# Kernel tuning notes

Hardware: AMD Instinct MI355X
Metric: run time of the kernel (lower is better)

## Reference

```python
import jax, jax.numpy as jnp
import numpy as np

B, T, H, V = 32, 256, 1024, 256


def setup_inputs() -> dict:
    key = jax.random.key(0)
    ks = jax.random.split(key, 12)
    xavier = float(np.sqrt(6.0 / (H + V)))
    inp = {
        "x": jax.random.randint(ks[0], (B, T), 0, V, dtype=jnp.int64),
        "targets": jax.random.randint(ks[1], (B, T), 0, V, dtype=jnp.int64),
        "h0": jnp.zeros((B, H), jnp.float32),
        "c0": jnp.zeros((B, H), jnp.float32),
        "h1": jnp.zeros((B, H), jnp.float32),
        "c1": jnp.zeros((B, H), jnp.float32),
        # learned params
        "emb": jax.random.normal(ks[2], (V, H), jnp.float32) * 0.05,
        "W_ih0": jax.random.normal(ks[3], (H, 4 * H), jnp.float32) / np.sqrt(H),
        "W_hh0": jax.random.normal(ks[4], (H, 4 * H), jnp.float32) / np.sqrt(H),
        "b0": jnp.zeros((4 * H,), jnp.float32),
        "W_ih1": jax.random.normal(ks[5], (H, 4 * H), jnp.float32) / np.sqrt(H),
        "W_hh1": jax.random.normal(ks[6], (H, 4 * H), jnp.float32) / np.sqrt(H),
        "b1": jnp.zeros((4 * H,), jnp.float32),
        "W_out": jax.random.uniform(ks[7], (H, V), jnp.float32, -xavier, xavier),
        "b_out": jnp.zeros((V,), jnp.float32),
    }
    return inp


def _lstm_cell(h, c, inp, W_ih, W_hh, b):
    # gates: [B, 4H] -> i, f, g, o
    z = inp @ W_ih + h @ W_hh + b
    i, f, g, o = jnp.split(z, 4, axis=-1)
    c_new = jax.nn.sigmoid(f) * c + jax.nn.sigmoid(i) * jnp.tanh(g)
    h_new = jax.nn.sigmoid(o) * jnp.tanh(c_new)
    return h_new, c_new


def reference(x, targets, h0, c0, h1, c1, emb, W_ih0, W_hh0, b0,
              W_ih1, W_hh1, b1, W_out, b_out):
    # Teacher-forcing branch: embed targets, feed embedding at every step.
    embeddings = emb[targets]            # [B, T, H]
    e_seq = jnp.swapaxes(embeddings, 0, 1)  # [T, B, H] for scan over time

    def step(carry, e_t):
        (h0, c0), (h1, c1) = carry
        h0, c0 = _lstm_cell(h0, c0, e_t, W_ih0, W_hh0, b0)
        h1, c1 = _lstm_cell(h1, c1, h0, W_ih1, W_hh1, b1)
        logit = h1 @ W_out + b_out       # [B, V]
        return ((h0, c0), (h1, c1)), logit

    carry0 = ((h0, c0), (h1, c1))
    carry_f, logits_tbv = jax.lax.scan(step, carry0, e_seq)
    logits = jnp.swapaxes(logits_tbv, 0, 1)  # [B, T, V]
    (h0f, c0f), (h1f, c1f) = carry_f
    return logits, h0f, c0f, h1f, c1f
```

## Files before the change

kernel.cpp:

```cpp
#include <hip/hip_runtime.h>
#include <cstdint>


typedef float    f32x4 __attribute__((ext_vector_type(4)));
typedef short    s16x8 __attribute__((ext_vector_type(8)));
typedef unsigned u32x4 __attribute__((ext_vector_type(4)));

#define DEV __device__ __forceinline__

DEV unsigned short f2bf(float x){
  unsigned u = __builtin_bit_cast(unsigned, x);
  unsigned r = (u + 0x7fffu + ((u >> 16) & 1u)) >> 16;
  return (unsigned short)r;
}
DEV float bf2f(unsigned short b){ return __builtin_bit_cast(float, ((unsigned)b) << 16); }

DEV s16x8 ld16(const void* p){ return *(const s16x8*)p; }

DEV f32x4 MF(s16x8 a, s16x8 b, f32x4 c){
  return __builtin_amdgcn_mfma_f32_16x16x32_bf16(a, b, c, 0, 0, 0);
}

#define LDC(dst, ptr)  asm volatile("global_load_dwordx4 %0, %1, off sc0 sc1" : "=v"(dst) : "v"(ptr))
#define LDP(dst, ptr)  asm volatile("global_load_dwordx4 %0, %1, off"         : "=v"(dst) : "v"(ptr))
#define WAITVM(n) do { asm volatile("s_waitcnt vmcnt(" #n ")" ::: "memory"); \
                       __builtin_amdgcn_sched_barrier(0); } while (0)
#define CFENCE()  asm volatile("" ::: "memory")
#define TRIPLE(Cmn, Ahm, Alm, Bhn, Bln) do { \
    Cmn = MF(Ahm, Bhn, Cmn); Cmn = MF(Ahm, Bln, Cmn); Cmn = MF(Alm, Bhn, Cmn); } while (0)

DEV void st16c(void* p, u32x4 v){
  asm volatile("global_store_dwordx4 %0, %1, off sc0 sc1" :: "v"(p), "v"(v) : "memory");
}
DEV void set_flag(int* p, int v){
  __hip_atomic_store(p, v, __ATOMIC_RELAXED, __HIP_MEMORY_SCOPE_AGENT);
}
template<int SLP>
DEV void pollT(const int* f, int lane, int target){
  const int* p0 = f + lane * 8;
  const int* p1 = f + (64 + lane) * 8;
  for (;;) {
    int a = __hip_atomic_load(p0, __ATOMIC_RELAXED, __HIP_MEMORY_SCOPE_AGENT);
    int b = __hip_atomic_load(p1, __ATOMIC_RELAXED, __HIP_MEMORY_SCOPE_AGENT);
    if (__all((a >= target) && (b >= target))) break;
    __builtin_amdgcn_s_sleep(SLP);
  }
  CFENCE();
}
DEV char* h0slot(char* wa0, char* s0, char* hi, int s){
  return (s == 0) ? s0 : ((s <= 128) ? wa0 + ((size_t)(s - 1) << 17)
                                     : hi  + ((size_t)(s - 129) << 17));
}

DEV void halfgemm8(const char* smemMat, const char* ALb, const char* Bb,
                   int wgl, int ksb, int lane, f32x4 (&C)[2][2]) {
  s16x8 P[3][4], AL[3][2];
  #pragma unroll
  for (int d = 0; d < 2; ++d) {
    #pragma unroll
    for (int q = 0; q < 4; ++q) LDP(P[d][q], Bb + ((q * 32 + ksb + d) << 10) + lane * 16);
    LDP(AL[d][0], ALb + ((((wgl * 2 + 0) * 2 + 1) * 32 + ksb + d) << 10) + lane * 16);
    LDP(AL[d][1], ALb + ((((wgl * 2 + 1) * 2 + 1) * 32 + ksb + d) << 10) + lane * 16);
  }
  #pragma unroll
  for (int i = 0; i < 8; ++i) {
    const int ks = ksb + i;
    if (i < 6) {
      #pragma unroll
      for (int q = 0; q < 4; ++q) LDP(P[(i + 2) % 3][q], Bb + ((q * 32 + ks + 2) << 10) + lane * 16);
      LDP(AL[(i + 2) % 3][0], ALb + ((((wgl * 2 + 0) * 2 + 1) * 32 + ks + 2) << 10) + lane * 16);
      LDP(AL[(i + 2) % 3][1], ALb + ((((wgl * 2 + 1) * 2 + 1) * 32 + ks + 2) << 10) + lane * 16);
    }
    s16x8 Ah0 = ld16(smemMat + ((0 * 32 + ks) << 10) + lane * 16);
    s16x8 Ah1 = ld16(smemMat + ((1 * 32 + ks) << 10) + lane * 16);
    if (i < 6) { WAITVM(12); } else if (i == 6) { WAITVM(6); } else { WAITVM(0); }
    TRIPLE(C[0][0], Ah0, AL[i % 3][0], P[i % 3][0], P[i % 3][2]);
    TRIPLE(C[0][1], Ah0, AL[i % 3][0], P[i % 3][1], P[i % 3][3]);
    TRIPLE(C[1][0], Ah1, AL[i % 3][1], P[i % 3][0], P[i % 3][2]);
    TRIPLE(C[1][1], Ah1, AL[i % 3][1], P[i % 3][1], P[i % 3][3]);
  }
}

__global__ void prep_wfrag(const float* __restrict__ W0, const float* __restrict__ W1,
                           const float* __restrict__ W2, const float* __restrict__ W3,
                           char* D0, char* D1, char* D2, char* D3) {
  int gid = blockIdx.x * 256 + threadIdx.x;
  int lane = gid & 63, ks = (gid >> 6) & 31, jb = (gid >> 11) & 255, mat = gid >> 19;
  const float* S = (mat == 0) ? W0 : (mat == 1) ? W1 : (mat == 2) ? W2 : W3;
  char* D = (mat == 0) ? D0 : (mat == 1) ? D1 : (mat == 2) ? D2 : D3;
  int jp = jb * 16 + (lane & 15), u = jp >> 2, g = jp & 3;
  int kb = ks * 32 + (lane >> 4) * 8;
  s16x8 vh, vl;
  #pragma unroll
  for (int i = 0; i < 8; ++i) {
    float x = S[(kb + i) * 4096 + g * 1024 + u];
    unsigned short h = f2bf(x);
    vh[i] = (short)h;
    vl[i] = (short)f2bf(x - bf2f(h));
  }
  *(s16x8*)(D + (((jb * 2 + 0) * 32 + ks) << 10) + lane * 16) = vh;
  *(s16x8*)(D + (((jb * 2 + 1) * 32 + ks) << 10) + lane * 16) = vl;
}

__global__ void prep_bfrag(const float* __restrict__ emb, const float* __restrict__ Wout,
                           char* Demb, char* Dwout) {
  int gid = blockIdx.x * 256 + threadIdx.x;
  int lane = gid & 63, ks = (gid >> 6) & 31, vb = (gid >> 11) & 15, which = gid >> 15;
  int v = vb * 16 + (lane & 15), kb = ks * 32 + (lane >> 4) * 8;
  s16x8 vh, vl;
  #pragma unroll
  for (int i = 0; i < 8; ++i) {
    float x = which ? Wout[(kb + i) * 256 + v] : emb[v * 1024 + kb + i];
    unsigned short h = f2bf(x);
    vh[i] = (short)h;
    vl[i] = (short)f2bf(x - bf2f(h));
  }
  char* D = which ? Dwout : Demb;
  *(s16x8*)(D + (((vb * 2 + 0) * 32 + ks) << 10) + lane * 16) = vh;
  *(s16x8*)(D + (((vb * 2 + 1) * 32 + ks) << 10) + lane * 16) = vl;
}

__global__ void prep_hinit(const float* __restrict__ h0, const float* __restrict__ h1,
                           char* h0s0, char* h1f) {
  int gid = blockIdx.x * 256 + threadIdx.x;
  int lane = gid & 63, ks = (gid >> 6) & 31, nt = (gid >> 11) & 1, which = gid >> 12;
  const float* S = which ? h1 : h0;
  char* D = which ? h1f : h0s0;
  int b = nt * 16 + (lane & 15), kb = ks * 32 + (lane >> 4) * 8;
  s16x8 vh, vl;
  #pragma unroll
  for (int i = 0; i < 8; ++i) {
    float x = S[b * 1024 + kb + i];
    unsigned short h = f2bf(x);
    vh[i] = (short)h;
    vl[i] = (short)f2bf(x - bf2f(h));
  }
  *(s16x8*)(D + (((0 * 2 + nt) * 32 + ks) << 10) + lane * 16) = vh;
  *(s16x8*)(D + (((1 * 2 + nt) * 32 + ks) << 10) + lane * 16) = vl;
}

__global__ void prep_misc(const float* __restrict__ b1, float* b1i, int* f0a, int* f1a) {
  int i = blockIdx.x * 256 + threadIdx.x;
  if (i < 4096) b1i[i] = b1[(i & 3) * 1024 + (i >> 2)];
  if (i < 1024) { f0a[i] = -1; f1a[i] = -1; }
}

__global__ __launch_bounds__(256, 1) void lstm_persist(
    const int* __restrict__ tgt,
    const float* __restrict__ c0_in, const float* __restrict__ c1_in,
    const float* __restrict__ b0, const float* __restrict__ b_out,
    char* __restrict__ WA0, const char* __restrict__ WA1, const char* __restrict__ WA2,
    const char* __restrict__ WAi0, const char* __restrict__ WoutB, const char* __restrict__ embB,
    float* __restrict__ E0, const float* __restrict__ b1i,
    char* __restrict__ h0s0, char* __restrict__ h0hi, char* __restrict__ h1frag,
    int* __restrict__ f0, int* __restrict__ f1,
    float* __restrict__ out)
{
  extern __shared__ char smem[];
  constexpr int PART = 131072;
  constexpr int RP   = 131072 + 16384;
  const int tid = threadIdx.x, lane = tid & 63, wv = tid >> 6;
  const int wg = blockIdx.x;
  const bool isL0 = (wg < 128);
  const int wgl = isL0 ? wg : (wg - 128);
  const int l15 = lane & 15, l4 = lane >> 4;
  const int mi_e = wv >> 1, nt_e = wv & 1;

  __builtin_amdgcn_fence(__ATOMIC_ACQUIRE, "agent");

  if (isL0) {
    u32x4 tmp[8];
    for (int blk = 0; blk < 4; ++blk) {
      #pragma unroll
      for (int q = 0; q < 8; ++q) {
        int idx = tid + (blk * 8 + q) * 256;
        int l16 = idx & 63, ks = (idx >> 6) & 31, mi = (idx >> 11) & 1, part = idx >> 12;
        LDC(tmp[q], WA0 + ((((wgl * 2 + mi) * 2 + part) * 32 + ks) << 10) + l16 * 16);
      }
      WAITVM(0);
      #pragma unroll
      for (int q = 0; q < 8; ++q) {
        int idx = tid + (blk * 8 + q) * 256;
        int l16 = idx & 63, ks = (idx >> 6) & 31, mi = (idx >> 11) & 1, part = idx >> 12;
        *(u32x4*)(smem + (((part * 2 + mi) * 32 + ks) << 10) + l16 * 16) = tmp[q];
      }
    }
  } else {
    for (int idx = tid; idx < 8192; idx += 256) {
      int l16 = idx & 63, ks = (idx >> 6) & 31, mi = (idx >> 11) & 1, mat = idx >> 12;
      const char* W = mat ? WA2 : WA1;
      u32x4 v = *(const u32x4*)(W + ((((wgl * 2 + mi) * 2 + 0) * 32 + ks) << 10) + l16 * 16);
      *(u32x4*)(smem + (((mat * 2 + mi) * 32 + ks) << 10) + l16 * 16) = v;
    }
  }

  if (isL0) {
    f32x4 C[2][4];
    #pragma unroll
    for (int a = 0; a < 2; ++a)
      #pragma unroll
      for (int b = 0; b < 4; ++b) C[a][b] = 0.0f;
    for (int ks = 0; ks < 32; ++ks) {
      s16x8 Ah0, Ah1, Al0, Al1;
      LDC(Ah0, WAi0 + ((((wgl * 2 + 0) * 2 + 0) * 32 + ks) << 10) + lane * 16);
      LDC(Ah1, WAi0 + ((((wgl * 2 + 1) * 2 + 0) * 32 + ks) << 10) + lane * 16);
      LDC(Al0, WAi0 + ((((wgl * 2 + 0) * 2 + 1) * 32 + ks) << 10) + lane * 16);
      LDC(Al1, WAi0 + ((((wgl * 2 + 1) * 2 + 1) * 32 + ks) << 10) + lane * 16);
      WAITVM(0);
      #pragma unroll
      for (int v4 = 0; v4 < 4; ++v4) {
        int vb = wv * 4 + v4;
        s16x8 Bh = ld16(embB + (((vb * 2 + 0) * 32 + ks) << 10) + lane * 16);
        s16x8 Bl = ld16(embB + (((vb * 2 + 1) * 32 + ks) << 10) + lane * 16);
        TRIPLE(C[0][v4], Ah0, Al0, Bh, Bl);
        TRIPLE(C[1][v4], Ah1, Al1, Bh, Bl);
      }
    }
    #pragma unroll
    for (int mi = 0; mi < 2; ++mi) {
      int jb4 = wgl * 32 + mi * 16 + l4 * 4;
      int u = jb4 >> 2;
      f32x4 bb;
      #pragma unroll
      for (int r = 0; r < 4; ++r) bb[r] = b0[r * 1024 + u];
      #pragma unroll
      for (int v4 = 0; v4 < 4; ++v4) {
        int v = (wv * 4 + v4) * 16 + l15;
        *(f32x4*)(E0 + v * 4096 + jb4) = C[mi][v4] + bb;
      }
    }
  }

  float cst;
  {
    const float* cs = isL0 ? c0_in : c1_in;
    cst = cs[(nt_e * 16 + l15) * 1024 + wgl * 8 + mi_e * 4 + l4];
  }
  f32x4 b1z = {0.f, 0.f, 0.f, 0.f};
  if (!isL0) b1z = *(const f32x4*)(b1i + wgl * 32 + mi_e * 16 + (l4 << 2));

  __syncthreads();
  if (tid == 0) set_flag((isL0 ? f0 : f1) + wgl * 8, 0);

  if (isL0) {
    for (int t = 0; t < 256; ++t) {
      const int s = t + 1;
      f32x4 C[2][2];
      #pragma unroll
      for (int a = 0; a < 2; ++a)
        #pragma unroll
        for (int b = 0; b < 2; ++b) C[a][b] = 0.0f;

      int tv = tgt[(nt_e * 16 + l15) * 256 + t];
      f32x4 e0v = *(const f32x4*)(E0 + (size_t)tv * 4096 + wgl * 32 + mi_e * 16 + (l4 << 2));
      pollT<1>(f0, lane, t);
      const char* Bb = h0slot(WA0, h0s0, h0hi, t);
      const int ksb = wv * 8;
      s16x8 P[3][4];
      #pragma unroll
      for (int d = 0; d < 2; ++d)
        #pragma unroll
        for (int q = 0; q < 4; ++q) LDP(P[d][q], Bb + ((q * 32 + ksb + d) << 10) + lane * 16);
      #pragma unroll
      for (int i = 0; i < 8; ++i) {
        const int ks = ksb + i;
        if (i < 6) {
          #pragma unroll
          for (int q = 0; q < 4; ++q) LDP(P[(i + 2) % 3][q], Bb + ((q * 32 + ks + 2) << 10) + lane * 16);
        }
        s16x8 Ah0 = ld16(smem + ((0 * 32 + ks) << 10) + lane * 16);
        s16x8 Ah1 = ld16(smem + ((1 * 32 + ks) << 10) + lane * 16);
        s16x8 Al0 = ld16(smem + ((2 * 32 + ks) << 10) + lane * 16);
        s16x8 Al1 = ld16(smem + ((3 * 32 + ks) << 10) + lane * 16);
        if (i < 6) { WAITVM(8); } else if (i == 6) { WAITVM(4); } else { WAITVM(0); }
        TRIPLE(C[0][0], Ah0, Al0, P[i % 3][0], P[i % 3][2]);
        TRIPLE(C[0][1], Ah0, Al0, P[i % 3][1], P[i % 3][3]);
        TRIPLE(C[1][0], Ah1, Al1, P[i % 3][0], P[i % 3][2]);
        TRIPLE(C[1][1], Ah1, Al1, P[i % 3][1], P[i % 3][3]);
      }

      #pragma unroll
      for (int mi = 0; mi < 2; ++mi)
        #pragma unroll
        for (int nt = 0; nt < 2; ++nt)
          *(f32x4*)(smem + PART + ((wv * 4 + mi * 2 + nt) << 10) + lane * 16) = C[mi][nt];
      __syncthreads();

      {
        f32x4 z = *(const f32x4*)(smem + PART + ((0 * 4 + wv) << 10) + lane * 16);
        #pragma unroll
        for (int w = 1; w < 4; ++w)
          z += *(const f32x4*)(smem + PART + ((w * 4 + wv) << 10) + lane * 16);
        z += e0v;
        float ig = 1.f / (1.f + __expf(-z[0]));
        float fg = 1.f / (1.f + __expf(-z[1]));
        float og = 1.f / (1.f + __expf(-z[3]));
        float cn = fg * cst + ig * tanhf(z[2]);
        float hn = og * tanhf(cn);
        cst = cn;
        unsigned short hb = f2bf(hn);
        unsigned short lb = f2bf(hn - bf2f(hb));
        *(short*)(smem + RP + ((0 + nt_e) * 16 + l15) * 16 + (mi_e * 4 + l4) * 2) = (short)hb;
        *(short*)(smem + RP + ((2 + nt_e) * 16 + l15) * 16 + (mi_e * 4 + l4) * 2) = (short)lb;
        if (t == 255) {
          int u = wgl * 8 + mi_e * 4 + l4, b = nt_e * 16 + l15;
          out[2097152 + b * 1024 + u] = hn;
          out[2097152 + 32768 + b * 1024 + u] = cn;
        }
      }
      __syncthreads();

      if (wv == 0) {
        char* hd = h0slot(WA0, h0s0, h0hi, s);
        u32x4 v = *(const u32x4*)(smem + RP + lane * 16);
        char* dst = hd + (((lane >> 4) * 32 + (wgl >> 2)) << 10) + ((wgl & 3) * 16 + l15) * 16;
        st16c(dst, v);
        asm volatile("s_waitcnt vmcnt(0)" ::: "memory");
        if (lane == 0) set_flag(f0 + wgl * 8, s);
      }
    }
  } else {
    f32x4 zpre;
    {
      pollT<2>(f0, lane, 1);
      f32x4 C2[2][2];
      #pragma unroll
      for (int a = 0; a < 2; ++a)
        #pragma unroll
        for (int b = 0; b < 2; ++b) C2[a][b] = 0.0f;
      halfgemm8(smem, WA1, h0slot(WA0, h0s0, h0hi, 1), wgl, wv * 8, lane, C2);
      #pragma unroll
      for (int mi = 0; mi < 2; ++mi)
        #pragma unroll
        for (int nt = 0; nt < 2; ++nt)
          *(f32x4*)(smem + PART + ((wv * 4 + mi * 2 + nt) << 10) + lane * 16) = C2[mi][nt];
      __syncthreads();
      zpre = *(const f32x4*)(smem + PART + ((0 * 4 + wv) << 10) + lane * 16);
      #pragma unroll
      for (int w = 1; w < 4; ++w)
        zpre += *(const f32x4*)(smem + PART + ((w * 4 + wv) << 10) + lane * 16);
      __syncthreads();
    }

    for (int t = 0; t < 256; ++t) {
      const int s = t + 1;
      f32x4 C[2][2];
      #pragma unroll
      for (int a = 0; a < 2; ++a)
        #pragma unroll
        for (int b = 0; b < 2; ++b) C[a][b] = 0.0f;

      pollT<1>(f1, lane, t);
      halfgemm8(smem + 65536, WA2, h1frag + (size_t)t * 131072, wgl, wv * 8, lane, C);

      #pragma unroll
      for (int mi = 0; mi < 2; ++mi)
        #pragma unroll
        for (int nt = 0; nt < 2; ++nt)
          *(f32x4*)(smem + PART + ((wv * 4 + mi * 2 + nt) << 10) + lane * 16) = C[mi][nt];
      __syncthreads();

      {
        f32x4 z = *(const f32x4*)(smem + PART + ((0 * 4 + wv) << 10) + lane * 16);
        #pragma unroll
        for (int w = 1; w < 4; ++w)
          z += *(const f32x4*)(smem + PART + ((w * 4 + wv) << 10) + lane * 16);
        z += zpre + b1z;
        float ig = 1.f / (1.f + __expf(-z[0]));
        float fg = 1.f / (1.f + __expf(-z[1]));
        float og = 1.f / (1.f + __expf(-z[3]));
        float cn = fg * cst + ig * tanhf(z[2]);
        float hn = og * tanhf(cn);
        cst = cn;
        unsigned short hb = f2bf(hn);
        unsigned short lb = f2bf(hn - bf2f(hb));
        *(short*)(smem + RP + ((0 + nt_e) * 16 + l15) * 16 + (mi_e * 4 + l4) * 2) = (short)hb;
        *(short*)(smem + RP + ((2 + nt_e) * 16 + l15) * 16 + (mi_e * 4 + l4) * 2) = (short)lb;
        if (t == 255) {
          int u = wgl * 8 + mi_e * 4 + l4, b = nt_e * 16 + l15;
          out[2097152 + 65536 + b * 1024 + u] = hn;
          out[2097152 + 65536 + 32768 + b * 1024 + u] = cn;
        }
      }
      __syncthreads();

      if (wv == 0) {
        char* hd = h1frag + (size_t)s * 131072;
        u32x4 v = *(const u32x4*)(smem + RP + lane * 16);
        char* dst = hd + (((lane >> 4) * 32 + (wgl >> 2)) << 10) + ((wgl & 3) * 16 + l15) * 16;
        st16c(dst, v);
        asm volatile("s_waitcnt vmcnt(0)" ::: "memory");
        if (lane == 0) set_flag(f1 + wgl * 8, s);
      }

      if (t < 255) {
        pollT<2>(f0, lane, t + 2);
        f32x4 C2[2][2];
        #pragma unroll
        for (int a = 0; a < 2; ++a)
          #pragma unroll
          for (int b = 0; b < 2; ++b) C2[a][b] = 0.0f;
        halfgemm8(smem, WA1, h0slot(WA0, h0s0, h0hi, t + 2), wgl, wv * 8, lane, C2);
        #pragma unroll
        for (int mi = 0; mi < 2; ++mi)
          #pragma unroll
          for (int nt = 0; nt < 2; ++nt)
            *(f32x4*)(smem + PART + ((wv * 4 + mi * 2 + nt) << 10) + lane * 16) = C2[mi][nt];
        __syncthreads();
        zpre = *(const f32x4*)(smem + PART + ((0 * 4 + wv) << 10) + lane * 16);
        #pragma unroll
        for (int w = 1; w < 4; ++w)
          zpre += *(const f32x4*)(smem + PART + ((w * 4 + wv) << 10) + lane * 16);
        __syncthreads();
      }
    }
  }

  {
    const int tp = isL0 ? wgl : (128 + wgl);
    pollT<32>(f1, lane, tp + 1);
    const char* A = h1frag + (size_t)(tp + 1) * 131072;
    f32x4 C[2][4];
    #pragma unroll
    for (int a = 0; a < 2; ++a)
      #pragma unroll
      for (int b = 0; b < 4; ++b) C[a][b] = 0.0f;
    s16x8 QA[4], QB[4];
    #pragma unroll
    for (int q = 0; q < 4; ++q) LDP(QA[q], A + ((q * 32 + 0) << 10) + lane * 16);
    for (int kk = 0; kk < 16; ++kk) {
      const int ks = kk * 2;
      #pragma unroll
      for (int q = 0; q < 4; ++q) LDP(QB[q], A + ((q * 32 + ks + 1) << 10) + lane * 16);
      asm volatile("s_waitcnt vmcnt(4)" ::: "memory");
      __builtin_amdgcn_sched_barrier(0);
      #pragma unroll
      for (int v4 = 0; v4 < 4; ++v4) {
        int vb = wv * 4 + v4;
        s16x8 Bh = ld16(WoutB + (((vb * 2 + 0) * 32 + ks) << 10) + lane * 16);
        s16x8 Bl = ld16(WoutB + (((vb * 2 + 1) * 32 + ks) << 10) + lane * 16);
        C[0][v4] = MF(QA[0], Bh, C[0][v4]); C[0][v4] = MF(QA[0], Bl, C[0][v4]); C[0][v4] = MF(QA[2], Bh, C[0][v4]);
        C[1][v4] = MF(QA[1], Bh, C[1][v4]); C[1][v4] = MF(QA[1], Bl, C[1][v4]); C[1][v4] = MF(QA[3], Bh, C[1][v4]);
      }
      if (kk < 15) {
        #pragma unroll
        for (int q = 0; q < 4; ++q) LDP(QA[q], A + ((q * 32 + ks + 2) << 10) + lane * 16);
        asm volatile("s_waitcnt vmcnt(4)" ::: "memory");
      } else {
        asm volatile("s_waitcnt vmcnt(0)" ::: "memory");
      }
      __builtin_amdgcn_sched_barrier(0);
      #pragma unroll
      for (int v4 = 0; v4 < 4; ++v4) {
        int vb = wv * 4 + v4;
        s16x8 Bh = ld16(WoutB + (((vb * 2 + 0) * 32 + ks + 1) << 10) + lane * 16);
        s16x8 Bl = ld16(WoutB + (((vb * 2 + 1) * 32 + ks + 1) << 10) + lane * 16);
        C[0][v4] = MF(QB[0], Bh, C[0][v4]); C[0][v4] = MF(QB[0], Bl, C[0][v4]); C[0][v4] = MF(QB[2], Bh, C[0][v4]);
        C[1][v4] = MF(QB[1], Bh, C[1][v4]); C[1][v4] = MF(QB[1], Bl, C[1][v4]); C[1][v4] = MF(QB[3], Bh, C[1][v4]);
      }
    }
    #pragma unroll
    for (int nt = 0; nt < 2; ++nt)
      #pragma unroll
      for (int v4 = 0; v4 < 4; ++v4) {
        int v = (wv * 4 + v4) * 16 + l15;
        float bo = b_out[v];
        #pragma unroll
        for (int r = 0; r < 4; ++r) {
          int b = nt * 16 + l4 * 4 + r;
          out[((size_t)b * 256 + tp) * 256 + v] = C[nt][v4][r] + bo;
        }
      }
  }
}

extern "C" void kernel_launch(void* const* d_in, const int* in_sizes, int n_in,
                              void* d_out, int out_size, void* d_ws, size_t ws_size,
                              hipStream_t stream) {
  const int*   targets = (const int*)d_in[1];
  const float* h0_in   = (const float*)d_in[2];
  const float* c0_in   = (const float*)d_in[3];
  const float* h1_in   = (const float*)d_in[4];
  const float* c1_in   = (const float*)d_in[5];
  const float* emb     = (const float*)d_in[6];
  const float* W_ih0   = (const float*)d_in[7];
  const float* W_hh0   = (const float*)d_in[8];
  const float* b0      = (const float*)d_in[9];
  const float* W_ih1   = (const float*)d_in[10];
  const float* W_hh1   = (const float*)d_in[11];
  const float* b1      = (const float*)d_in[12];
  const float* W_out   = (const float*)d_in[13];
  const float* b_out   = (const float*)d_in[14];
  float* out = (float*)d_out;

  char* ws = (char*)d_ws;
  char*  WA0    = ws;
  char*  WA1    = ws + 16777216;
  char*  WA2    = ws + 33554432;
  char*  WoutB  = ws + 50331648;
  char*  embB   = ws + 51380224;
  float* E0     = (float*)(ws + 52428800);
  float* b1i    = (float*)(ws + 56623104);
  int*   f0     = (int*)(ws + 56639488);
  int*   f1     = (int*)(ws + 56643584);
  char*  h0s0   = ws + 56647680;
  char*  h0hi   = ws + 56778752;
  char*  h1frag = ws + 73555968;
  char*  WAi0   = h1frag + 16777216;

  prep_misc <<<18,   256, 0, stream>>>(b1, b1i, f0, f1);
  prep_wfrag<<<8192, 256, 0, stream>>>(W_hh0, W_ih1, W_hh1, W_ih0, WA0, WA1, WA2, WAi0);
  prep_bfrag<<<256,  256, 0, stream>>>(emb, W_out, embB, WoutB);
  prep_hinit<<<32,   256, 0, stream>>>(h0_in, h1_in, h0s0, h1frag);

  hipFuncSetAttribute(reinterpret_cast<const void*>(lstm_persist),
                      hipFuncAttributeMaxDynamicSharedMemorySize, 148480);
  lstm_persist<<<256, 256, 148480, stream>>>(
      targets, c0_in, c1_in, b0, b_out,
      WA0, WA1, WA2, WAi0, WoutB, embB,
      E0, b1i, h0s0, h0hi, h1frag, f0, f1, out);
}
```

Baseline: 1.729 ms.

## Split layer-1 into separate input-projection and recurrent workgroup groups with ring buffer

Layer-1 work previously done by 128 workgroups is split into two groups of 64. One group computes the W_ih1·h0 projection and pushes partial gate sums into a 4-slot global ring. The other group computes the W_hh1·h1 recurrence, adds the ring entry and runs the cell update. Each workgroup now handles 16 gate rows via a wider gemm16u, and a new flag array f2 plus combined polls coordinate the stages. The aim is to take the input projection off the layer-1 recurrent critical path. In exchange it adds global traffic for the ring, more cross-workgroup polling, and serialises the activation step on a single wave.

```diff
diff --git a/kernel.cpp b/kernel.cpp
--- a/kernel.cpp
+++ b/kernel.cpp
@@ -32,6 +32,7 @@
 DEV void st16c(void* p, u32x4 v){
   asm volatile("global_store_dwordx4 %0, %1, off sc0 sc1" :: "v"(p), "v"(v) : "memory");
 }
+DEV void st16cf(void* p, f32x4 v){ st16c(p, __builtin_bit_cast(u32x4, v)); }
 DEV void set_flag(int* p, int v){
   __hip_atomic_store(p, v, __ATOMIC_RELAXED, __HIP_MEMORY_SCOPE_AGENT);
 }
@@ -47,20 +48,48 @@
   }
   CFENCE();
 }
+DEV void pollC(const int* f1p, int t1, const int* f2p, int t2, int lane){
+  const int* a = f1p + lane * 8;
+  const int* b = f2p + lane * 8;
+  for (;;) {
+    int x = __hip_atomic_load(a, __ATOMIC_RELAXED, __HIP_MEMORY_SCOPE_AGENT);
+    int y = __hip_atomic_load(b, __ATOMIC_RELAXED, __HIP_MEMORY_SCOPE_AGENT);
+    if (__all((x >= t1) && (y >= t2))) break;
+    __builtin_amdgcn_s_sleep(1);
+  }
+  CFENCE();
+}
+DEV void pollB(const int* f0p, int t0, const int* f2p, int t2,
+               const int* f1p, int t1, int lane){
+  const int* a0 = f0p + lane * 8;
+  const int* a1 = f0p + (64 + lane) * 8;
+  const int* b  = f2p + lane * 8;
+  const int* c  = f1p + lane * 8;
+  for (;;) {
+    int x0 = __hip_atomic_load(a0, __ATOMIC_RELAXED, __HIP_MEMORY_SCOPE_AGENT);
+    int x1 = __hip_atomic_load(a1, __ATOMIC_RELAXED, __HIP_MEMORY_SCOPE_AGENT);
+    int y  = __hip_atomic_load(b,  __ATOMIC_RELAXED, __HIP_MEMORY_SCOPE_AGENT);
+    int z  = __hip_atomic_load(c,  __ATOMIC_RELAXED, __HIP_MEMORY_SCOPE_AGENT);
+    if (__all((x0 >= t0) && (x1 >= t0) && (y >= t2) && (z >= t1))) break;
+    __builtin_amdgcn_s_sleep(2);
+  }
+  CFENCE();
+}
 DEV char* h0slot(char* wa0, char* s0, char* hi, int s){
   return (s == 0) ? s0 : ((s <= 128) ? wa0 + ((size_t)(s - 1) << 17)
                                      : hi  + ((size_t)(s - 129) << 17));
 }
 
-DEV void halfgemm8(const char* smemMat, const char* ALb, const char* Bb,
-                   int wgl, int ksb, int lane, f32x4 (&C)[2][2]) {
-  s16x8 P[3][4], AL[3][2];
+DEV void gemm16u(const char* smemA, const char* ALb, int jb0, const char* Bb,
+                 int ksb, int lane, f32x4 (&C)[4][2]) {
+  s16x8 P[3][4], AL[3][4];
   #pragma unroll
   for (int d = 0; d < 2; ++d) {
     #pragma unroll
     for (int q = 0; q < 4; ++q) LDP(P[d][q], Bb + ((q * 32 + ksb + d) << 10) + lane * 16);
-    LDP(AL[d][0], ALb + ((((wgl * 2 + 0) * 2 + 1) * 32 + ksb + d) << 10) + lane * 16);
-    LDP(AL[d][1], ALb + ((((wgl * 2 + 1) * 2 + 1) * 32 + ksb + d) << 10) + lane * 16);
+    #pragma unroll
+    for (int m = 0; m < 4; ++m)
+      LDP(AL[d][m], ALb + ((((jb0 + m) * 2 + 1) * 32 + ksb + d) << 10) + lane * 16);
   }
   #pragma unroll
   for (int i = 0; i < 8; ++i) {
@@ -68,16 +97,19 @@
     if (i < 6) {
       #pragma unroll
       for (int q = 0; q < 4; ++q) LDP(P[(i + 2) % 3][q], Bb + ((q * 32 + ks + 2) << 10) + lane * 16);
-      LDP(AL[(i + 2) % 3][0], ALb + ((((wgl * 2 + 0) * 2 + 1) * 32 + ks + 2) << 10) + lane * 16);
-      LDP(AL[(i + 2) % 3][1], ALb + ((((wgl * 2 + 1) * 2 + 1) * 32 + ks + 2) << 10) + lane * 16);
-    }
-    s16x8 Ah0 = ld16(smemMat + ((0 * 32 + ks) << 10) + lane * 16);
-    s16x8 Ah1 = ld16(smemMat + ((1 * 32 + ks) << 10) + lane * 16);
-    if (i < 6) { WAITVM(12); } else if (i == 6) { WAITVM(6); } else { WAITVM(0); }
-    TRIPLE(C[0][0], Ah0, AL[i % 3][0], P[i % 3][0], P[i % 3][2]);
-    TRIPLE(C[0][1], Ah0, AL[i % 3][0], P[i % 3][1], P[i % 3][3]);
-    TRIPLE(C[1][0], Ah1, AL[i % 3][1], P[i % 3][0], P[i % 3][2]);
-    TRIPLE(C[1][1], Ah1, AL[i % 3][1], P[i % 3][1], P[i % 3][3]);
+      #pragma unroll
+      for (int m = 0; m < 4; ++m)
+        LDP(AL[(i + 2) % 3][m], ALb + ((((jb0 + m) * 2 + 1) * 32 + ks + 2) << 10) + lane * 16);
+    }
+    s16x8 Ah[4];
+    #pragma unroll
+    for (int m = 0; m < 4; ++m) Ah[m] = ld16(smemA + ((m * 32 + ks) << 10) + lane * 16);
+    if (i < 6) { WAITVM(16); } else if (i == 6) { WAITVM(8); } else { WAITVM(0); }
+    #pragma unroll
+    for (int m = 0; m < 4; ++m) {
+      TRIPLE(C[m][0], Ah[m], AL[i % 3][m], P[i % 3][0], P[i % 3][2]);
+      TRIPLE(C[m][1], Ah[m], AL[i % 3][m], P[i % 3][1], P[i % 3][3]);
+    }
   }
 }
 
@@ -139,10 +171,15 @@
   *(s16x8*)(D + (((1 * 2 + nt) * 32 + ks) << 10) + lane * 16) = vl;
 }
 
-__global__ void prep_misc(const float* __restrict__ b1, float* b1i, int* f0a, int* f1a) {
+__global__ void prep_misc(const float* __restrict__ b1, float* b1i,
+                          int* f0a, int* f1a, int* f2a) {
   int i = blockIdx.x * 256 + threadIdx.x;
   if (i < 4096) b1i[i] = b1[(i & 3) * 1024 + (i >> 2)];
-  if (i < 1024) { f0a[i] = -1; f1a[i] = -1; }
+  if (i < 1024) {
+    f0a[i] = -1;
+    f1a[i] = (i >= 512) ? 0x7fffffff : -1;
+    f2a[i] = (i >= 512) ? 0x7fffffff : -1;
+  }
 }
 
 __global__ __launch_bounds__(256, 1) void lstm_persist(
@@ -153,96 +190,82 @@
     const char* __restrict__ WAi0, const char* __restrict__ WoutB, const char* __restrict__ embB,
     float* __restrict__ E0, const float* __restrict__ b1i,
     char* __restrict__ h0s0, char* __restrict__ h0hi, char* __restrict__ h1frag,
-    int* __restrict__ f0, int* __restrict__ f1,
+    char* __restrict__ z1ring,
+    int* __restrict__ f0, int* __restrict__ f1, int* __restrict__ f2,
     float* __restrict__ out)
 {
   extern __shared__ char smem[];
-  constexpr int PART = 131072;
-  constexpr int RP   = 131072 + 16384;
+  constexpr int PARTA = 131072;
+  constexpr int RP0   = 147456;
+  constexpr int PARTB = 131072;
+  constexpr int RP1   = 155648;
   const int tid = threadIdx.x, lane = tid & 63, wv = tid >> 6;
   const int wg = blockIdx.x;
-  const bool isL0 = (wg < 128);
-  const int wgl = isL0 ? wg : (wg - 128);
   const int l15 = lane & 15, l4 = lane >> 4;
-  const int mi_e = wv >> 1, nt_e = wv & 1;
 
   __builtin_amdgcn_fence(__ATOMIC_ACQUIRE, "agent");
 
-  if (isL0) {
-    u32x4 tmp[8];
-    for (int blk = 0; blk < 4; ++blk) {
-      #pragma unroll
-      for (int q = 0; q < 8; ++q) {
-        int idx = tid + (blk * 8 + q) * 256;
-        int l16 = idx & 63, ks = (idx >> 6) & 31, mi = (idx >> 11) & 1, part = idx >> 12;
-        LDC(tmp[q], WA0 + ((((wgl * 2 + mi) * 2 + part) * 32 + ks) << 10) + l16 * 16);
-      }
-      WAITVM(0);
-      #pragma unroll
-      for (int q = 0; q < 8; ++q) {
-        int idx = tid + (blk * 8 + q) * 256;
-        int l16 = idx & 63, ks = (idx >> 6) & 31, mi = (idx >> 11) & 1, part = idx >> 12;
-        *(u32x4*)(smem + (((part * 2 + mi) * 32 + ks) << 10) + l16 * 16) = tmp[q];
-      }
-    }
-  } else {
-    for (int idx = tid; idx < 8192; idx += 256) {
-      int l16 = idx & 63, ks = (idx >> 6) & 31, mi = (idx >> 11) & 1, mat = idx >> 12;
-      const char* W = mat ? WA2 : WA1;
-      u32x4 v = *(const u32x4*)(W + ((((wgl * 2 + mi) * 2 + 0) * 32 + ks) << 10) + l16 * 16);
-      *(u32x4*)(smem + (((mat * 2 + mi) * 32 + ks) << 10) + l16 * 16) = v;
-    }
-  }
-
-  if (isL0) {
-    f32x4 C[2][4];
-    #pragma unroll
-    for (int a = 0; a < 2; ++a)
-      #pragma unroll
-      for (int b = 0; b < 4; ++b) C[a][b] = 0.0f;
-    for (int ks = 0; ks < 32; ++ks) {
-      s16x8 Ah0, Ah1, Al0, Al1;
-      LDC(Ah0, WAi0 + ((((wgl * 2 + 0) * 2 + 0) * 32 + ks) << 10) + lane * 16);
-      LDC(Ah1, WAi0 + ((((wgl * 2 + 1) * 2 + 0) * 32 + ks) << 10) + lane * 16);
-      LDC(Al0, WAi0 + ((((wgl * 2 + 0) * 2 + 1) * 32 + ks) << 10) + lane * 16);
-      LDC(Al1, WAi0 + ((((wgl * 2 + 1) * 2 + 1) * 32 + ks) << 10) + lane * 16);
-      WAITVM(0);
-      #pragma unroll
-      for (int v4 = 0; v4 < 4; ++v4) {
-        int vb = wv * 4 + v4;
-        s16x8 Bh = ld16(embB + (((vb * 2 + 0) * 32 + ks) << 10) + lane * 16);
-        s16x8 Bl = ld16(embB + (((vb * 2 + 1) * 32 + ks) << 10) + lane * 16);
-        TRIPLE(C[0][v4], Ah0, Al0, Bh, Bl);
-        TRIPLE(C[1][v4], Ah1, Al1, Bh, Bl);
-      }
-    }
-    #pragma unroll
-    for (int mi = 0; mi < 2; ++mi) {
-      int jb4 = wgl * 32 + mi * 16 + l4 * 4;
-      int u = jb4 >> 2;
-      f32x4 bb;
-      #pragma unroll
-      for (int r = 0; r < 4; ++r) bb[r] = b0[r * 1024 + u];
-      #pragma unroll
-      for (int v4 = 0; v4 < 4; ++v4) {
-        int v = (wv * 4 + v4) * 16 + l15;
-        *(f32x4*)(E0 + v * 4096 + jb4) = C[mi][v4] + bb;
-      }
-    }
-  }
-
-  float cst;
-  {
-    const float* cs = isL0 ? c0_in : c1_in;
-    cst = cs[(nt_e * 16 + l15) * 1024 + wgl * 8 + mi_e * 4 + l4];
-  }
-  f32x4 b1z = {0.f, 0.f, 0.f, 0.f};
-  if (!isL0) b1z = *(const f32x4*)(b1i + wgl * 32 + mi_e * 16 + (l4 << 2));
-
-  __syncthreads();
-  if (tid == 0) set_flag((isL0 ? f0 : f1) + wgl * 8, 0);
-
-  if (isL0) {
+  if (wg < 128) {
+    const int wgl = wg;
+    const int mi_e = wv >> 1, nt_e = wv & 1;
+    {
+      u32x4 tmp[8];
+      for (int blk = 0; blk < 4; ++blk) {
+        #pragma unroll
+        for (int q = 0; q < 8; ++q) {
+          int idx = tid + (blk * 8 + q) * 256;
+          int l16 = idx & 63, ks = (idx >> 6) & 31, mi = (idx >> 11) & 1, part = idx >> 12;
+          LDC(tmp[q], WA0 + ((((wgl * 2 + mi) * 2 + part) * 32 + ks) << 10) + l16 * 16);
+        }
+        WAITVM(0);
+        #pragma unroll
+        for (int q = 0; q < 8; ++q) {
+          int idx = tid + (blk * 8 + q) * 256;
+          int l16 = idx & 63, ks = (idx >> 6) & 31, mi = (idx >> 11) & 1, part = idx >> 12;
+          *(u32x4*)(smem + (((part * 2 + mi) * 32 + ks) << 10) + l16 * 16) = tmp[q];
+        }
+      }
+    }
+    {
+      f32x4 C[2][4];
+      #pragma unroll
+      for (int a = 0; a < 2; ++a)
+        #pragma unroll
+        for (int b = 0; b < 4; ++b) C[a][b] = 0.0f;
+      for (int ks = 0; ks < 32; ++ks) {
+        s16x8 Ah0, Ah1, Al0, Al1;
+        LDC(Ah0, WAi0 + ((((wgl * 2 + 0) * 2 + 0) * 32 + ks) << 10) + lane * 16);
+        LDC(Ah1, WAi0 + ((((wgl * 2 + 1) * 2 + 0) * 32 + ks) << 10) + lane * 16);
+        LDC(Al0, WAi0 + ((((wgl * 2 + 0) * 2 + 1) * 32 + ks) << 10) + lane * 16);
+        LDC(Al1, WAi0 + ((((wgl * 2 + 1) * 2 + 1) * 32 + ks) << 10) + lane * 16);
+        WAITVM(0);
+        #pragma unroll
+        for (int v4 = 0; v4 < 4; ++v4) {
+          int vb = wv * 4 + v4;
+          s16x8 Bh = ld16(embB + (((vb * 2 + 0) * 32 + ks) << 10) + lane * 16);
+          s16x8 Bl = ld16(embB + (((vb * 2 + 1) * 32 + ks) << 10) + lane * 16);
+          TRIPLE(C[0][v4], Ah0, Al0, Bh, Bl);
+          TRIPLE(C[1][v4], Ah1, Al1, Bh, Bl);
+        }
+      }
+      #pragma unroll
+      for (int mi = 0; mi < 2; ++mi) {
+        int jb4 = wgl * 32 + mi * 16 + l4 * 4;
+        int u = jb4 >> 2;
+        f32x4 bb;
+        #pragma unroll
+        for (int r = 0; r < 4; ++r) bb[r] = b0[r * 1024 + u];
+        #pragma unroll
+        for (int v4 = 0; v4 < 4; ++v4) {
+          int v = (wv * 4 + v4) * 16 + l15;
+          *(f32x4*)(E0 + v * 4096 + jb4) = C[mi][v4] + bb;
+        }
+      }
+    }
+    float cst = c0_in[(nt_e * 16 + l15) * 1024 + wgl * 8 + mi_e * 4 + l4];
+    __syncthreads();
+    if (tid == 0) set_flag(f0 + wgl * 8, 0);
+
     for (int t = 0; t < 256; ++t) {
       const int s = t + 1;
       f32x4 C[2][2];
@@ -250,7 +273,6 @@
       for (int a = 0; a < 2; ++a)
         #pragma unroll
         for (int b = 0; b < 2; ++b) C[a][b] = 0.0f;
-
       int tv = tgt[(nt_e * 16 + l15) * 256 + t];
       f32x4 e0v = *(const f32x4*)(E0 + (size_t)tv * 4096 + wgl * 32 + mi_e * 16 + (l4 << 2));
       pollT<1>(f0, lane, t);
@@ -278,19 +300,17 @@
         TRIPLE(C[1][0], Ah1, Al1, P[i % 3][0], P[i % 3][2]);
         TRIPLE(C[1][1], Ah1, Al1, P[i % 3][1], P[i % 3][3]);
       }
-
       #pragma unroll
       for (int mi = 0; mi < 2; ++mi)
         #pragma unroll
         for (int nt = 0; nt < 2; ++nt)
-          *(f32x4*)(smem + PART + ((wv * 4 + mi * 2 + nt) << 10) + lane * 16) = C[mi][nt];
+          *(f32x4*)(smem + PARTA + ((wv * 4 + mi * 2 + nt) << 10) + lane * 16) = C[mi][nt];
       __syncthreads();
-
       {
-        f32x4 z = *(const f32x4*)(smem + PART + ((0 * 4 + wv) << 10) + lane * 16);
+        f32x4 z = *(const f32x4*)(smem + PARTA + ((0 * 4 + wv) << 10) + lane * 16);
         #pragma unroll
         for (int w = 1; w < 4; ++w)
-          z += *(const f32x4*)(smem + PART + ((w * 4 + wv) << 10) + lane * 16);
+          z += *(const f32x4*)(smem + PARTA + ((w * 4 + wv) << 10) + lane * 16);
         z += e0v;
         float ig = 1.f / (1.f + __expf(-z[0]));
         float fg = 1.f / (1.f + __expf(-z[1]));
@@ -300,8 +320,8 @@
         cst = cn;
         unsigned short hb = f2bf(hn);
         unsigned short lb = f2bf(hn - bf2f(hb));
-        *(short*)(smem + RP + ((0 + nt_e) * 16 + l15) * 16 + (mi_e * 4 + l4) * 2) = (short)hb;
-        *(short*)(smem + RP + ((2 + nt_e) * 16 + l15) * 16 + (mi_e * 4 + l4) * 2) = (short)lb;
+        *(short*)(smem + RP0 + ((0 + nt_e) * 16 + l15) * 16 + (mi_e * 4 + l4) * 2) = (short)hb;
+        *(short*)(smem + RP0 + ((2 + nt_e) * 16 + l15) * 16 + (mi_e * 4 + l4) * 2) = (short)lb;
         if (t == 255) {
           int u = wgl * 8 + mi_e * 4 + l4, b = nt_e * 16 + l15;
           out[2097152 + b * 1024 + u] = hn;
@@ -309,115 +329,154 @@
         }
       }
       __syncthreads();
-
       if (wv == 0) {
         char* hd = h0slot(WA0, h0s0, h0hi, s);
-        u32x4 v = *(const u32x4*)(smem + RP + lane * 16);
+        u32x4 v = *(const u32x4*)(smem + RP0 + lane * 16);
         char* dst = hd + (((lane >> 4) * 32 + (wgl >> 2)) << 10) + ((wgl & 3) * 16 + l15) * 16;
         st16c(dst, v);
         asm volatile("s_waitcnt vmcnt(0)" ::: "memory");
         if (lane == 0) set_flag(f0 + wgl * 8, s);
       }
     }
+  } else if (wg < 192) {
+    const int wgb = wg - 128;
+    const int jb0 = wgb * 4;
+    for (int idx = tid; idx < 8192; idx += 256) {
+      int l16 = idx & 63, ks = (idx >> 6) & 31, m = idx >> 11;
+      u32x4 v = *(const u32x4*)(WA1 + ((((jb0 + m) * 2 + 0) * 32 + ks) << 10) + l16 * 16);
+      *(u32x4*)(smem + ((m * 32 + ks) << 10) + l16 * 16) = v;
+    }
+    __syncthreads();
+    if (tid == 0) set_flag(f2 + wgb * 8, 0);
+
+    for (int t = 0; t < 256; ++t) {
+      const int rt = (t >= 4) ? (t - 3) : 0;
+      pollB(f0, t + 1, f2, t, f1, rt, lane);
+      f32x4 Cb[4][2];
+      #pragma unroll
+      for (int a = 0; a < 4; ++a)
+        #pragma unroll
+        for (int b = 0; b < 2; ++b) Cb[a][b] = 0.0f;
+      gemm16u(smem, WA1, jb0, h0slot(WA0, h0s0, h0hi, t + 1), wv * 8, lane, Cb);
+      if (wv) {
+        #pragma unroll
+        for (int m = 0; m < 4; ++m)
+          #pragma unroll
+          for (int n = 0; n < 2; ++n)
+            *(f32x4*)(smem + PARTB + (((wv - 1) * 8 + m * 2 + n) << 10) + lane * 16) = Cb[m][n];
+      }
+      __syncthreads();
+      if (wv == 0) {
+        char* zs = z1ring + ((size_t)(t & 3) * 64 + wgb) * 8192;
+        #pragma unroll
+        for (int m = 0; m < 4; ++m)
+          #pragma unroll
+          for (int n = 0; n < 2; ++n) {
+            f32x4 z = Cb[m][n];
+            #pragma unroll
+            for (int w = 1; w < 4; ++w)
+              z += *(const f32x4*)(smem + PARTB + (((w - 1) * 8 + m * 2 + n) << 10) + lane * 16);
+            st16cf(zs + ((m * 2 + n) * 64 + lane) * 16, z);
+          }
+        asm volatile("s_waitcnt vmcnt(0)" ::: "memory");
+        if (lane == 0) set_flag(f2 + wgb * 8, t + 1);
+      }
+    }
   } else {
-    f32x4 zpre;
-    {
-      pollT<2>(f0, lane, 1);
-      f32x4 C2[2][2];
-      #pragma unroll
-      for (int a = 0; a < 2; ++a)
-        #pragma unroll
-        for (int b = 0; b < 2; ++b) C2[a][b] = 0.0f;
-      halfgemm8(smem, WA1, h0slot(WA0, h0s0, h0hi, 1), wgl, wv * 8, lane, C2);
-      #pragma unroll
-      for (int mi = 0; mi < 2; ++mi)
-        #pragma unroll
-        for (int nt = 0; nt < 2; ++nt)
-          *(f32x4*)(smem + PART + ((wv * 4 + mi * 2 + nt) << 10) + lane * 16) = C2[mi][nt];
-      __syncthreads();
-      zpre = *(const f32x4*)(smem + PART + ((0 * 4 + wv) << 10) + lane * 16);
-      #pragma unroll
-      for (int w = 1; w < 4; ++w)
-        zpre += *(const f32x4*)(smem + PART + ((w * 4 + wv) << 10) + lane * 16);
-      __syncthreads();
-    }
+    const int wgc = wg - 192;
+    const int jb0 = wgc * 4;
+    for (int idx = tid; idx < 8192; idx += 256) {
+      int l16 = idx & 63, ks = (idx >> 6) & 31, m = idx >> 11;
+      u32x4 v = *(const u32x4*)(WA2 + ((((jb0 + m) * 2 + 0) * 32 + ks) << 10) + l16 * 16);
+      *(u32x4*)(smem + ((m * 32 + ks) << 10) + l16 * 16) = v;
+    }
+    f32x4 b1z4[4];
+    float cst[4][2];
+    if (wv == 0) {
+      #pragma unroll
+      for (int m = 0; m < 4; ++m) {
+        b1z4[m] = *(const f32x4*)(b1i + wgc * 64 + m * 16 + (l4 << 2));
+        #pragma unroll
+        for (int n = 0; n < 2; ++n)
+          cst[m][n] = c1_in[(n * 16 + l15) * 1024 + wgc * 16 + m * 4 + l4];
+      }
+    }
+    __syncthreads();
+    if (tid == 0) set_flag(f1 + wgc * 8, 0);
 
     for (int t = 0; t < 256; ++t) {
       const int s = t + 1;
-      f32x4 C[2][2];
-      #pragma unroll
-      for (int a = 0; a < 2; ++a)
-        #pragma unroll
-        for (int b = 0; b < 2; ++b) C[a][b] = 0.0f;
-
-      pollT<1>(f1, lane, t);
-      halfgemm8(smem + 65536, WA2, h1frag + (size_t)t * 131072, wgl, wv * 8, lane, C);
-
-      #pragma unroll
-      for (int mi = 0; mi < 2; ++mi)
-        #pragma unroll
-        for (int nt = 0; nt < 2; ++nt)
-          *(f32x4*)(smem + PART + ((wv * 4 + mi * 2 + nt) << 10) + lane * 16) = C[mi][nt];
+      pollC(f1, t, f2, s, lane);
+      f32x4 zA[4][2];
+      if (wv == 0) {
+        const char* zs = z1ring + ((size_t)(t & 3) * 64 + wgc) * 8192;
+        #pragma unroll
+        for (int m = 0; m < 4; ++m)
+          #pragma unroll
+          for (int n = 0; n < 2; ++n)
+            LDC(zA[m][n], zs + ((m * 2 + n) * 64 + lane) * 16);
+      }
+      f32x4 Cc[4][2];
+      #pragma unroll
+      for (int a = 0; a < 4; ++a)
+        #pragma unroll
+        for (int b = 0; b < 2; ++b) Cc[a][b] = 0.0f;
+      gemm16u(smem, WA2, jb0, h1frag + (size_t)t * 131072, wv * 8, lane, Cc);
+      if (wv) {
+        #pragma unroll
+        for (int m = 0; m < 4; ++m)
+          #pragma unroll
+          for (int n = 0; n < 2; ++n)
+            *(f32x4*)(smem + PARTB + (((wv - 1) * 8 + m * 2 + n) << 10) + lane * 16) = Cc[m][n];
+      }
       __syncthreads();
-
-      {
-        f32x4 z = *(const f32x4*)(smem + PART + ((0 * 4 + wv) << 10) + lane * 16);
-        #pragma unroll
-        for (int w = 1; w < 4; ++w)
-          z += *(const f32x4*)(smem + PART + ((w * 4 + wv) << 10) + lane * 16);
-        z += zpre + b1z;
-        float ig = 1.f / (1.f + __expf(-z[0]));
-        float fg = 1.f / (1.f + __expf(-z[1]));
-        float og = 1.f / (1.f + __expf(-z[3]));
-        float cn = fg * cst + ig * tanhf(z[2]);
-        float hn = og * tanhf(cn);
-        cst = cn;
-        unsigned short hb = f2bf(hn);
-        unsigned short lb = f2bf(hn - bf2f(hb));
-        *(short*)(smem + RP + ((0 + nt_e) * 16 + l15) * 16 + (mi_e * 4 + l4) * 2) = (short)hb;
-        *(short*)(smem + RP + ((2 + nt_e) * 16 + l15) * 16 + (mi_e * 4 + l4) * 2) = (short)lb;
-        if (t == 255) {
-          int u = wgl * 8 + mi_e * 4 + l4, b = nt_e * 16 + l15;
-          out[2097152 + 65536 + b * 1024 + u] = hn;
-          out[2097152 + 65536 + 32768 + b * 1024 + u] = cn;
-        }
-      }
-      __syncthreads();
-
       if (wv == 0) {
+        #pragma unroll
+        for (int m = 0; m < 4; ++m)
+          #pragma unroll
+          for (int n = 0; n < 2; ++n) {
+            f32x4 z = Cc[m][n];
+            #pragma unroll
+            for (int w = 1; w < 4; ++w)
+              z += *(const f32x4*)(smem + PARTB + (((w - 1) * 8 + m * 2 + n) << 10) + lane * 16);
+            z += zA[m][n] + b1z4[m];
+            float ig = 1.f / (1.f + __expf(-z[0]));
+            float fg = 1.f / (1.f + __expf(-z[1]));
+            float og = 1.f / (1.f + __expf(-z[3]));
+            float cn = fg * cst[m][n] + ig * tanhf(z[2]);
+            float hn = og * tanhf(cn);
+            cst[m][n] = cn;
+            unsigned short hb = f2bf(hn);
+            unsigned short lb = f2bf(hn - bf2f(hb));
+            int i8 = (m * 4 + l4) & 7, subl = (m * 4 + l4) >> 3;
+            *(short*)(smem + RP1 + (((0 * 2 + n) * 2 + subl) * 16 + l15) * 16 + i8 * 2) = (short)hb;
+            *(short*)(smem + RP1 + (((1 * 2 + n) * 2 + subl) * 16 + l15) * 16 + i8 * 2) = (short)lb;
+            if (t == 255) {
+              int u = wgc * 16 + m * 4 + l4, b = n * 16 + l15;
+              out[2097152 + 65536 + b * 1024 + u] = hn;
+              out[2097152 + 98304 + b * 1024 + u] = cn;
+            }
+          }
         char* hd = h1frag + (size_t)s * 131072;
-        u32x4 v = *(const u32x4*)(smem + RP + lane * 16);
-        char* dst = hd + (((lane >> 4) * 32 + (wgl >> 2)) << 10) + ((wgl & 3) * 16 + l15) * 16;
-        st16c(dst, v);
+        asm volatile("s_waitcnt lgkmcnt(0)" ::: "memory");
+        __builtin_amdgcn_sched_barrier(0);
+        #pragma unroll
+        for (int h = 0; h < 2; ++h) {
+          int idx16 = lane * 2 + h;
+          u32x4 v = *(const u32x4*)(smem + RP1 + idx16 * 16);
+          int l15r = idx16 & 15, subl = (idx16 >> 4) & 1, ntq = (idx16 >> 5) & 1, part = idx16 >> 6;
+          char* dst = hd + (((part * 2 + ntq) * 32 + (wgc >> 1)) << 10)
+                         + (((wgc & 1) * 2 + subl) * 16 + l15r) * 16;
+          st16c(dst, v);
+        }
         asm volatile("s_waitcnt vmcnt(0)" ::: "memory");
-        if (lane == 0) set_flag(f1 + wgl * 8, s);
-      }
-
-      if (t < 255) {
-        pollT<2>(f0, lane, t + 2);
-        f32x4 C2[2][2];
-        #pragma unroll
-        for (int a = 0; a < 2; ++a)
-          #pragma unroll
-          for (int b = 0; b < 2; ++b) C2[a][b] = 0.0f;
-        halfgemm8(smem, WA1, h0slot(WA0, h0s0, h0hi, t + 2), wgl, wv * 8, lane, C2);
-        #pragma unroll
-        for (int mi = 0; mi < 2; ++mi)
-          #pragma unroll
-          for (int nt = 0; nt < 2; ++nt)
-            *(f32x4*)(smem + PART + ((wv * 4 + mi * 2 + nt) << 10) + lane * 16) = C2[mi][nt];
-        __syncthreads();
-        zpre = *(const f32x4*)(smem + PART + ((0 * 4 + wv) << 10) + lane * 16);
-        #pragma unroll
-        for (int w = 1; w < 4; ++w)
-          zpre += *(const f32x4*)(smem + PART + ((w * 4 + wv) << 10) + lane * 16);
-        __syncthreads();
+        if (lane == 0) set_flag(f1 + wgc * 8, s);
       }
     }
   }
 
   {
-    const int tp = isL0 ? wgl : (128 + wgl);
+    const int tp = wg;
     pollT<32>(f1, lane, tp + 1);
     const char* A = h1frag + (size_t)(tp + 1) * 131072;
     f32x4 C[2][4];
@@ -506,17 +565,19 @@
   char*  h0s0   = ws + 56647680;
   char*  h0hi   = ws + 56778752;
   char*  h1frag = ws + 73555968;
+  char*  z1ring = ws + 107241472;
+  int*   f2     = (int*)(ws + 109338624);
   char*  WAi0   = h1frag + 16777216;
 
-  prep_misc <<<18,   256, 0, stream>>>(b1, b1i, f0, f1);
+  prep_misc <<<18,   256, 0, stream>>>(b1, b1i, f0, f1, f2);
   prep_wfrag<<<8192, 256, 0, stream>>>(W_hh0, W_ih1, W_hh1, W_ih0, WA0, WA1, WA2, WAi0);
   prep_bfrag<<<256,  256, 0, stream>>>(emb, W_out, embB, WoutB);
   prep_hinit<<<32,   256, 0, stream>>>(h0_in, h1_in, h0s0, h1frag);
 
   hipFuncSetAttribute(reinterpret_cast<const void*>(lstm_persist),
-                      hipFuncAttributeMaxDynamicSharedMemorySize, 148480);
-  lstm_persist<<<256, 256, 148480, stream>>>(
+                      hipFuncAttributeMaxDynamicSharedMemorySize, 157696);
+  lstm_persist<<<256, 256, 157696, stream>>>(
       targets, c0_in, c1_in, b0, b_out,
       WA0, WA1, WA2, WAi0, WoutB, embB,
-      E0, b1i, h0s0, h0hi, h1frag, f0, f1, out);
-}
+      E0, b1i, h0s0, h0hi, h1frag, z1ring, f0, f1, f2, out);
+}
```

Measured after the change: 2.106 ms. 1.22x slower.
